# Kernel optimization log

Hardware: AMD Instinct MI355X
Metric: run time of the kernel (lower is better)

The kernel has to match this reference:

```python
import jax, jax.numpy as jnp
import numpy as np

B, S, D, H, L = 8, 1024, 768, 12, 8
DH = D // H
V, NCOND, DPA, NACT = 1024, 256, 64, 4
COND = DPA * NACT  # 256


def setup_inputs() -> dict:
    key = jax.random.key(0)
    ks = jax.random.split(key, 24)
    s = 0.02
    return {
        "tokens": jax.random.randint(ks[0], (B, S), 0, V),
        "actions": jax.random.randint(ks[1], (B, NACT), 0, NCOND),
        "emb": jax.random.normal(ks[2], (V, D)) * s,
        "act_emb": jax.random.normal(ks[3], (NCOND, DPA)) * s,
        "ln1_g": jax.random.normal(ks[4], (L, COND, D)) * s,
        "ln1_b": jax.random.normal(ks[5], (L, COND, D)) * s,
        "Wq": jax.random.normal(ks[6], (L, H, DH, DH)) * s,
        "Wk": jax.random.normal(ks[7], (L, H, DH, DH)) * s,
        "Wv": jax.random.normal(ks[8], (L, H, DH, DH)) * s,
        "Wo": jax.random.normal(ks[9], (L, D, D)) * s,
        "bo": jnp.zeros((L, D)),
        "ln2_g": jax.random.normal(ks[10], (L, COND, D)) * s,
        "ln2_b": jax.random.normal(ks[11], (L, COND, D)) * s,
        "W1": jax.random.normal(ks[12], (L, D, 4 * D)) * s,
        "b1": jnp.zeros((L, 4 * D)),
        "W2": jax.random.normal(ks[13], (L, 4 * D, D)) * s,
        "b2": jnp.zeros((L, D)),
        "lnf_g": jax.random.normal(ks[14], (COND, D)) * s,
        "lnf_b": jax.random.normal(ks[15], (COND, D)) * s,
        "Wout": jax.random.normal(ks[16], (D, V)) * s,
        "bout": jnp.zeros((V,)),
    }


def _sinusoidal_pe():
    pos = jnp.arange(S, dtype=jnp.float32)[:, None]
    div = jnp.exp(jnp.arange(0, D, 2, dtype=jnp.float32) * (-np.log(10000.0) / D))
    pe = jnp.zeros((S, D))
    pe = pe.at[:, 0::2].set(jnp.sin(pos * div))
    pe = pe.at[:, 1::2].set(jnp.cos(pos * div))
    return pe


def _cond_ln(x, a, gw, bw, eps=1e-5):
    # affine-free layernorm, conditional gain/shift from action vector (VideoGPT-style CondLayerNorm)
    mu = x.mean(-1, keepdims=True)
    var = ((x - mu) ** 2).mean(-1, keepdims=True)
    h = (x - mu) * jax.lax.rsqrt(var + eps)
    g = a @ gw  # [B, D]
    b = a @ bw
    return h * g[:, None, :] + b[:, None, :]


def _attn(h, wq, wk, wv, wo, bo_):
    xh = h.reshape(B, S, H, DH)
    q = jnp.einsum("bshd,hde->bshe", xh, wq)
    k = jnp.einsum("bshd,hde->bshe", xh, wk)
    v = jnp.einsum("bshd,hde->bshe", xh, wv)
    logits = jnp.einsum("bshe,bthe->bhst", q, k) / np.sqrt(DH)  # d_model per head = DH
    p = jax.nn.softmax(logits, axis=-1)
    o = jnp.einsum("bhst,bthd->bshd", p, v).reshape(B, S, D)
    return o @ wo + bo_


def reference(tokens, actions, emb, act_emb, ln1_g, ln1_b, Wq, Wk, Wv, Wo, bo,
              ln2_g, ln2_b, W1, b1, W2, b2, lnf_g, lnf_b, Wout, bout):
    x = emb[tokens] + _sinusoidal_pe()[None]  # [B, S, D]
    a = act_emb[actions].reshape(B, -1)  # first_action_only -> [B, COND]
    for l in range(L):
        h = _cond_ln(x, a, ln1_g[l], ln1_b[l])
        x = x + _attn(h, Wq[l], Wk[l], Wv[l], Wo[l], bo[l])
        h = _cond_ln(x, a, ln2_g[l], ln2_b[l])
        h = jax.nn.gelu(h @ W1[l] + b1[l]) @ W2[l] + b2[l]
        x = x + h
    x = _cond_ln(x, a, lnf_g, lnf_b)
    return x @ Wout + bout
```

## Files before the change

kernel.cpp:

```cpp
#include <hip/hip_runtime.h>
#include <hip/hip_bf16.h>

typedef unsigned short u16;
typedef __attribute__((ext_vector_type(8))) short bf16x8;
typedef __attribute__((ext_vector_type(4))) float f32x4;

#define NB 8
#define NS 1024
#define ND 768
#define NH 12
#define NL 8
#define NDH 64
#define NV 1024
#define NCONDV 256
#define NTOK (NB*NS)

union BF8 { bf16x8 v; u16 u[8]; };
union US4 { ushort4 v; u16 u[4]; };

__device__ __forceinline__ float b2f(u16 u){ return __uint_as_float(((unsigned)u) << 16); }
__device__ __forceinline__ u16 f2b(float f){
  unsigned u = __float_as_uint(f);
  return (u16)((u + 0x7fffu + ((u >> 16) & 1u)) >> 16);
}

__device__ __forceinline__ void glds16(const u16* g, u16* l) {
  __builtin_amdgcn_global_load_lds((const __attribute__((address_space(1))) void*)g,
                                   (__attribute__((address_space(3))) void*)l, 16, 0, 0);
}

#define MEMFENCE asm volatile("" ::: "memory")

__global__ __launch_bounds__(256) void k_embed(const int* __restrict__ tokens,
                                               const float* __restrict__ emb,
                                               float* __restrict__ x)
{
  const int t = blockIdx.x;
  const int s = t & (NS - 1);
  const int tok = tokens[t];
  const float c = (float)(-9.210340371976184 / 768.0);
  for (int d = threadIdx.x; d < ND; d += 256) {
    float div = expf((float)(d & ~1) * c);
    float ang = (float)s * div;
    float pe = (d & 1) ? cosf(ang) : sinf(ang);
    x[(size_t)t*ND + d] = emb[(size_t)tok*ND + d] + pe;
  }
}

__global__ __launch_bounds__(256) void k_actvec(const int* __restrict__ actions,
                                                const float* __restrict__ act_emb,
                                                float* __restrict__ a)
{
  const int b = blockIdx.x, j = threadIdx.x;
  const int i = j >> 6, kk = j & 63;
  const int act = actions[b*4 + i];
  a[b*NCONDV + j] = act_emb[(size_t)act*64 + kk];
}

__global__ __launch_bounds__(256) void k_gains(const float* __restrict__ a,
    const float* __restrict__ g1, const float* __restrict__ b1,
    const float* __restrict__ g2, const float* __restrict__ b2,
    const float* __restrict__ gf, const float* __restrict__ bfp,
    float* __restrict__ outp)
{
  __shared__ float sa[NB*NCONDV];
  const int m = blockIdx.x, dc = blockIdx.y;
  for (int i = threadIdx.x; i < NB*NCONDV; i += 256) sa[i] = a[i];
  __syncthreads();
  const float* W;
  if (m < 32) {
    int ll = m >> 2, w = m & 3;
    const float* base = (w==0) ? g1 : (w==1) ? b1 : (w==2) ? g2 : b2;
    W = base + (size_t)ll * NCONDV * ND;
  } else {
    W = (m == 32) ? gf : bfp;
  }
  const int d = dc*256 + threadIdx.x;
  float acc[NB] = {0,0,0,0,0,0,0,0};
  for (int j = 0; j < NCONDV; j++) {
    float w = W[(size_t)j*ND + d];
    #pragma unroll
    for (int bb = 0; bb < NB; bb++) acc[bb] += sa[bb*NCONDV + j] * w;
  }
  #pragma unroll
  for (int bb = 0; bb < NB; bb++) outp[((size_t)m*NB + bb)*ND + d] = acc[bb];
}

__global__ __launch_bounds__(256) void k_cln(const float* __restrict__ x,
                                             const float* __restrict__ g,
                                             const float* __restrict__ bb,
                                             u16* __restrict__ h)
{
  const int tid = threadIdx.x, w = tid >> 6, lane = tid & 63;
  const int t = blockIdx.x*4 + w;
  const int bi = t >> 10;
  const float* xr = x + (size_t)t*ND;
  f32x4 v0 = *(const f32x4*)(xr + lane*4);
  f32x4 v1 = *(const f32x4*)(xr + 256 + lane*4);
  f32x4 v2 = *(const f32x4*)(xr + 512 + lane*4);
  float s = (v0[0]+v0[1]+v0[2]+v0[3]) + (v1[0]+v1[1]+v1[2]+v1[3]) + (v2[0]+v2[1]+v2[2]+v2[3]);
  #pragma unroll
  for (int off = 1; off < 64; off <<= 1) s += __shfl_xor(s, off);
  float mu = s * (1.0f/768.0f);
  float s2 = 0.f;
  #pragma unroll
  for (int i = 0; i < 4; i++) { v0[i] -= mu; s2 += v0[i]*v0[i]; }
  #pragma unroll
  for (int i = 0; i < 4; i++) { v1[i] -= mu; s2 += v1[i]*v1[i]; }
  #pragma unroll
  for (int i = 0; i < 4; i++) { v2[i] -= mu; s2 += v2[i]*v2[i]; }
  #pragma unroll
  for (int off = 1; off < 64; off <<= 1) s2 += __shfl_xor(s2, off);
  float rs = rsqrtf(s2 * (1.0f/768.0f) + 1e-5f);
  const float* gr = g + (size_t)bi*ND;
  const float* br = bb + (size_t)bi*ND;
  u16* hr = h + (size_t)t*ND;
  #pragma unroll
  for (int j = 0; j < 3; j++) {
    f32x4 vv = (j==0) ? v0 : (j==1) ? v1 : v2;
    f32x4 gg = *(const f32x4*)(gr + j*256 + lane*4);
    f32x4 bv = *(const f32x4*)(br + j*256 + lane*4);
    US4 o;
    #pragma unroll
    for (int i = 0; i < 4; i++) o.u[i] = f2b(vv[i]*rs*gg[i] + bv[i]);
    *(ushort4*)(hr + j*256 + lane*4) = o.v;
  }
}

__global__ __launch_bounds__(256) void k_wprep(const float* __restrict__ src,
                                               u16* __restrict__ dst, int K, int N)
{
  __shared__ u16 t[64][65];
  const int k0 = blockIdx.x*64, n0 = blockIdx.y*64;
  const size_t mz = (size_t)blockIdx.z * K * N;
  src += mz; dst += mz;
  {
    int r = threadIdx.x >> 2, c0 = (threadIdx.x & 3) * 16;
    const float* s = src + (size_t)(k0 + r)*N + n0 + c0;
    f32x4 a = *(const f32x4*)s, b = *(const f32x4*)(s+4);
    f32x4 c = *(const f32x4*)(s+8), d = *(const f32x4*)(s+12);
    #pragma unroll
    for (int i = 0; i < 4; i++) {
      t[r][c0+i]    = f2b(a[i]);
      t[r][c0+4+i]  = f2b(b[i]);
      t[r][c0+8+i]  = f2b(c[i]);
      t[r][c0+12+i] = f2b(d[i]);
    }
  }
  __syncthreads();
  {
    int rn = threadIdx.x >> 2, kc = (threadIdx.x & 3)*16;
    u16* dp = dst + (size_t)(n0+rn)*K + k0 + kc;
    BF8 o0, o1;
    #pragma unroll
    for (int i = 0; i < 8; i++) { o0.u[i] = t[kc+i][rn]; o1.u[i] = t[kc+8+i][rn]; }
    *(bf16x8*)dp = o0.v; *(bf16x8*)(dp+8) = o1.v;
  }
}

__global__ __launch_bounds__(256) void k_qkv(const u16* __restrict__ h,
    const float* __restrict__ Wq, const float* __restrict__ Wk, const float* __restrict__ Wv,
    u16* __restrict__ qo, u16* __restrict__ ko, u16* __restrict__ vo)
{
  __shared__ alignas(16) u16 wlds[64][72];
  const int t0 = blockIdx.x * 64, head = blockIdx.y, which = blockIdx.z;
  const float* W = ((which==0) ? Wq : (which==1) ? Wk : Wv) + (size_t)head*NDH*NDH;
  {
    int d = threadIdx.x >> 2, e0 = (threadIdx.x & 3) * 16;
    const float* wr = W + (size_t)d*NDH + e0;
    f32x4 f0 = *(const f32x4*)wr;
    f32x4 f1 = *(const f32x4*)(wr + 4);
    f32x4 f2 = *(const f32x4*)(wr + 8);
    f32x4 f3 = *(const f32x4*)(wr + 12);
    #pragma unroll
    for (int i = 0; i < 4; i++) {
      wlds[e0+i][d]    = f2b(f0[i]);
      wlds[e0+4+i][d]  = f2b(f1[i]);
      wlds[e0+8+i][d]  = f2b(f2[i]);
      wlds[e0+12+i][d] = f2b(f3[i]);
    }
  }
  __syncthreads();
  const int wave = threadIdx.x >> 6, lane = threadIdx.x & 63;
  const int lo16 = lane & 15, quad = lane >> 4;
  const int arow = t0 + wave*16 + lo16;
  const u16* hr = h + (size_t)arow*ND + head*NDH + quad*8;
  bf16x8 a0 = *(const bf16x8*)hr;
  bf16x8 a1 = *(const bf16x8*)(hr + 32);
  f32x4 acc[4] = {{0,0,0,0},{0,0,0,0},{0,0,0,0},{0,0,0,0}};
  #pragma unroll
  for (int n = 0; n < 4; n++) {
    const u16* bp = &wlds[n*16 + lo16][quad*8];
    bf16x8 b0 = *(const bf16x8*)bp;
    bf16x8 b1 = *(const bf16x8*)(bp + 32);
    acc[n] = __builtin_amdgcn_mfma_f32_16x16x32_bf16(a0, b0, acc[n], 0, 0, 0);
    acc[n] = __builtin_amdgcn_mfma_f32_16x16x32_bf16(a1, b1, acc[n], 0, 0, 0);
  }
  #pragma unroll
  for (int n = 0; n < 4; n++) {
    #pragma unroll
    for (int r = 0; r < 4; r++) {
      int t = t0 + wave*16 + quad*4 + r;
      int bb = t >> 10, s = t & (NS-1);
      int e = n*16 + lo16;
      u16 val = f2b(acc[n][r]);
      if (which == 2) {
        int local = s & 127;
        int col = (s & ~127) | (((local & 15) << 3) | (local >> 4));
        vo[(((size_t)bb*NH + head)*NDH + e)*NS + col] = val;
      } else {
        u16* dst = (which == 0) ? qo : ko;
        dst[(((size_t)bb*NH + head)*NS + s)*NDH + e] = val;
      }
    }
  }
}

__global__ __launch_bounds__(256) void k_attn2(const u16* __restrict__ q,
                                               const u16* __restrict__ kk,
                                               const u16* __restrict__ vt,
                                               u16* __restrict__ o)
{
  __shared__ alignas(16) u16 klds[128][72];
  __shared__ alignas(16) u16 vlds[64][136];
  __shared__ alignas(16) u16 plds[4][16][136];
  const int tid = threadIdx.x, w = tid >> 6, lane = tid & 63;
  const int lo16 = lane & 15, quad = lane >> 4;
  const int bh = blockIdx.x;
  const int b = bh / NH, head = bh - b*NH;
  const int q0 = blockIdx.y*64 + w*16;
  const u16* qb = q  + (size_t)bh*NS*NDH;
  const u16* kb = kk + (size_t)bh*NS*NDH;
  const u16* vb = vt + (size_t)bh*NDH*NS;
  BF8 aq0, aq1;
  {
    const u16* qr = qb + (size_t)(q0 + lo16)*NDH + quad*8;
    BF8 r0, r1; r0.v = *(const bf16x8*)qr; r1.v = *(const bf16x8*)(qr + 32);
    const float qs = 0.125f * 1.44269504088896f;
    #pragma unroll
    for (int j = 0; j < 8; j++) {
      aq0.u[j] = f2b(b2f(r0.u[j]) * qs);
      aq1.u[j] = f2b(b2f(r1.u[j]) * qs);
    }
  }
  float lsum[4] = {0,0,0,0};
  f32x4 oacc[4] = {{0,0,0,0},{0,0,0,0},{0,0,0,0},{0,0,0,0}};

  bf16x8 kreg[4], vreg[4];
  #pragma unroll
  for (int i = 0; i < 4; i++) {
    int c = tid + 256*i;
    kreg[i] = *(const bf16x8*)(kb + (size_t)(c>>3)*NDH + (c&7)*8);
    vreg[i] = *(const bf16x8*)(vb + (size_t)(c>>4)*NS + (c&15)*8);
  }

  for (int kt = 0; kt < NS; kt += 128) {
    __syncthreads();
    #pragma unroll
    for (int i = 0; i < 4; i++) {
      int c = tid + 256*i;
      *(bf16x8*)&klds[c>>3][(c&7)*8] = kreg[i];
      *(bf16x8*)&vlds[c>>4][(c&15)*8] = vreg[i];
    }
    __syncthreads();
    if (kt + 128 < NS) {
      #pragma unroll
      for (int i = 0; i < 4; i++) {
        int c = tid + 256*i;
        kreg[i] = *(const bf16x8*)(kb + (size_t)(kt + 128 + (c>>3))*NDH + (c&7)*8);
        vreg[i] = *(const bf16x8*)(vb + (size_t)(c>>4)*NS + (kt + 128) + (c&15)*8);
      }
    }
    f32x4 s[8];
    #pragma unroll
    for (int j = 0; j < 8; j++) {
      const u16* kr = &klds[j*16 + lo16][quad*8];
      bf16x8 b0 = *(const bf16x8*)kr;
      bf16x8 b1 = *(const bf16x8*)(kr + 32);
      f32x4 z = {0,0,0,0};
      z = __builtin_amdgcn_mfma_f32_16x16x32_bf16(aq0.v, b0, z, 0, 0, 0);
      s[j] = __builtin_amdgcn_mfma_f32_16x16x32_bf16(aq1.v, b1, z, 0, 0, 0);
    }
    #pragma unroll
    for (int r = 0; r < 4; r++) {
      float p[8];
      #pragma unroll
      for (int j = 0; j < 8; j++) p[j] = exp2f(s[j][r]);
      unsigned pk32[4];
      #pragma unroll
      for (int j = 0; j < 4; j++)
        asm("v_cvt_pk_bf16_f32 %0, %1, %2" : "=v"(pk32[j]) : "v"(p[2*j]), "v"(p[2*j+1]));
      float ps = 0.f;
      #pragma unroll
      for (int j = 0; j < 4; j++) {
        ps += __uint_as_float(pk32[j] << 16);
        ps += __uint_as_float(pk32[j] & 0xffff0000u);
      }
      lsum[r] += ps;
      union { unsigned u[4]; bf16x8 v; } pkv;
      #pragma unroll
      for (int j = 0; j < 4; j++) pkv.u[j] = pk32[j];
      *(bf16x8*)&plds[w][quad*4 + r][lo16*8] = pkv.v;
    }
    #pragma unroll
    for (int kc = 0; kc < 4; kc++) {
      bf16x8 pa = *(const bf16x8*)&plds[w][lo16][kc*32 + quad*8];
      #pragma unroll
      for (int n = 0; n < 4; n++) {
        bf16x8 vf = *(const bf16x8*)&vlds[n*16 + lo16][kc*32 + quad*8];
        oacc[n] = __builtin_amdgcn_mfma_f32_16x16x32_bf16(pa, vf, oacc[n], 0, 0, 0);
      }
    }
  }
  #pragma unroll
  for (int r = 0; r < 4; r++) {
    #pragma unroll
    for (int off = 1; off < 16; off <<= 1) lsum[r] += __shfl_xor(lsum[r], off);
  }
  #pragma unroll
  for (int n = 0; n < 4; n++) {
    #pragma unroll
    for (int r = 0; r < 4; r++) {
      int s_ = q0 + quad*4 + r;
      int d = head*NDH + n*16 + lo16;
      o[((size_t)b*NS + s_)*ND + d] = f2b(oacc[n][r] / lsum[r]);
    }
  }
}

template<int EPI>
__global__ __launch_bounds__(512) void k_gemm3(
    const u16* __restrict__ A, const u16* __restrict__ Bt,
    const float* __restrict__ bias, const float* __restrict__ resid,
    void* __restrict__ out, int M, int N, int K)
{
  extern __shared__ u16 lds[];
  const int tid = threadIdx.x;
  const int lane = tid & 63, lo16 = lane & 15, quad = lane >> 4;
  const int w = tid >> 6;
  const int wm = (w & 3) << 6;
  const int wn = (w >> 2) << 6;

  const int nwg = (int)gridDim.x, flat = (int)blockIdx.x;
  const int swzid = (flat & 7) * (nwg >> 3) + (flat >> 3);
  const int nbn = N >> 7;
  const int mb = swzid / nbn, nb = swzid - mb*nbn;
  const int m0 = mb << 8, n0 = nb << 7;
  const int NT = K >> 6;

  const int sr = tid >> 3, ss = tid & 7;
  const int sg = ((ss ^ (sr & 7)) << 3);
  const u16* Asrc = A + (size_t)(m0 + sr) * K + sg;
  const u16* Bsrc = Bt + (size_t)(n0 + sr) * K + sg;
  const size_t K64 = (size_t)K << 6;
  u16* const sd = lds + tid * 8;

  const int sw0 = ((quad ^ (lo16 & 7)) << 3);
  const int sw1 = (((4 + quad) ^ (lo16 & 7)) << 3);
  const int arow = (wm + lo16) << 6;
  const int brow = (wn + lo16) << 6;

  f32x4 acc[4][4];
  #pragma unroll
  for (int i = 0; i < 4; i++)
    #pragma unroll
    for (int j = 0; j < 4; j++) acc[i][j] = (f32x4){0,0,0,0};

  auto STAGE = [&](int t, int bi) {
    u16* dst = sd + bi * 24576;
    const size_t ko = (size_t)t << 6;
    #pragma unroll
    for (int c = 0; c < 4; c++) glds16(Asrc + ko + (size_t)c*K64, dst + c*4096);
    #pragma unroll
    for (int c = 0; c < 2; c++) glds16(Bsrc + ko + (size_t)c*K64, dst + 16384 + c*4096);
  };

  STAGE(0, 0);
  if (NT > 1) STAGE(1, 1);

  int cu = 0;
  for (int t = 0; t < NT; t++) {
    const int st = (cu == 0) ? 2 : cu - 1;
    MEMFENCE; __builtin_amdgcn_s_barrier(); MEMFENCE;
    if (t + 2 < NT) {
      STAGE(t + 2, st);
      asm volatile("s_waitcnt vmcnt(12)" ::: "memory");
    } else if (t + 1 < NT) {
      asm volatile("s_waitcnt vmcnt(6)" ::: "memory");
    } else {
      asm volatile("s_waitcnt vmcnt(0)" ::: "memory");
    }
    MEMFENCE; __builtin_amdgcn_s_barrier(); MEMFENCE;
    const u16* cb = lds + cu * 24576;
    bf16x8 af[4][2], bf[4][2];
    #pragma unroll
    for (int mf = 0; mf < 4; mf++) {
      af[mf][0] = *(const bf16x8*)(cb + arow + mf*1024 + sw0);
      af[mf][1] = *(const bf16x8*)(cb + arow + mf*1024 + sw1);
    }
    #pragma unroll
    for (int nf = 0; nf < 4; nf++) {
      bf[nf][0] = *(const bf16x8*)(cb + 16384 + brow + nf*1024 + sw0);
      bf[nf][1] = *(const bf16x8*)(cb + 16384 + brow + nf*1024 + sw1);
    }
    __builtin_amdgcn_s_setprio(1);
    #pragma unroll
    for (int kk = 0; kk < 2; kk++)
      #pragma unroll
      for (int mf = 0; mf < 4; mf++)
        #pragma unroll
        for (int nf = 0; nf < 4; nf++)
          acc[mf][nf] = __builtin_amdgcn_mfma_f32_16x16x32_bf16(af[mf][kk], bf[nf][kk], acc[mf][nf], 0, 0, 0);
    __builtin_amdgcn_s_setprio(0);
    cu = (cu == 2) ? 0 : cu + 1;
  }

  #pragma unroll
  for (int mf = 0; mf < 4; mf++) {
    #pragma unroll
    for (int nf = 0; nf < 4; nf++) {
      const int col = n0 + wn + nf*16 + lo16;
      const float bv = bias[col];
      #pragma unroll
      for (int r = 0; r < 4; r++) {
        const int row = m0 + wm + mf*16 + quad*4 + r;
        const size_t idx = (size_t)row * N + col;
        float v = acc[mf][nf][r] + bv;
        if (EPI == 1) {
          float u = 0.7978845608028654f*(v + 0.044715f*v*v*v);
          float e = __expf(2.0f*u);
          float th = (e - 1.0f) / (e + 1.0f);
          ((u16*)out)[idx] = f2b(0.5f*v*(1.0f + th));
        } else if (EPI == 2) {
          ((float*)out)[idx] = v + resid[idx];
        } else {
          ((float*)out)[idx] = v;
        }
      }
    }
  }
}

template<int EPI, int MT>
__global__ __launch_bounds__(256) void k_gemm_t(
    const u16* __restrict__ A, const u16* __restrict__ Bt,
    const float* __restrict__ bias, const float* resid,
    void* out, int M, int N, int K)
{
  constexpr int MI = MT/32;
  __shared__ alignas(16) u16 alds[2*MT*32];
  __shared__ alignas(16) u16 blds[2*128*32];
  const int m0 = blockIdx.x*MT, n0 = blockIdx.y*128;
  const int tid = threadIdx.x;
  const int w = tid >> 6, lane = tid & 63, lo16 = lane & 15, quad = lane >> 4;
  const int wm = (w & 1)*(MT/2), wn = (w >> 1)*64;
  f32x4 acc[MI][4];
  #pragma unroll
  for (int i = 0; i < MI; i++)
    #pragma unroll
    for (int j = 0; j < 4; j++) acc[i][j] = (f32x4){0,0,0,0};
  const int r0 = tid >> 2, c0 = (tid & 3)*8;
  const u16* Ap = A  + (size_t)(m0 + r0)*K + c0;
  const u16* Bp = Bt + (size_t)(n0 + r0)*K + c0;
  for (int k0 = 0; k0 < K; k0 += 64) {
    __syncthreads();
    #pragma unroll
    for (int h = 0; h < 2; h++) {
      const int ho = h*32;
      glds16(Ap + k0 + ho, alds + h*(MT*32) + tid*8);
      if (MT == 128) glds16(Ap + (size_t)64*K + k0 + ho, alds + h*(MT*32) + 2048 + tid*8);
      glds16(Bp + k0 + ho, blds + h*4096 + tid*8);
      glds16(Bp + (size_t)64*K + k0 + ho, blds + h*4096 + 2048 + tid*8);
    }
    __syncthreads();
    #pragma unroll
    for (int h = 0; h < 2; h++) {
      const u16* ah = alds + h*(MT*32);
      const u16* bh = blds + h*4096;
      bf16x8 af[MI], bf[4];
      #pragma unroll
      for (int i = 0; i < MI; i++) af[i] = *(const bf16x8*)&ah[(wm + i*16 + lo16)*32 + quad*8];
      #pragma unroll
      for (int j = 0; j < 4; j++) bf[j] = *(const bf16x8*)&bh[(wn + j*16 + lo16)*32 + quad*8];
      #pragma unroll
      for (int i = 0; i < MI; i++)
        #pragma unroll
        for (int j = 0; j < 4; j++)
          acc[i][j] = __builtin_amdgcn_mfma_f32_16x16x32_bf16(af[i], bf[j], acc[i][j], 0, 0, 0);
    }
  }
  #pragma unroll
  for (int j = 0; j < 4; j++) {
    int col = n0 + wn + j*16 + lo16;
    float bv = bias[col];
    #pragma unroll
    for (int i = 0; i < MI; i++) {
      #pragma unroll
      for (int r = 0; r < 4; r++) {
        int row = m0 + wm + i*16 + quad*4 + r;
        float v = acc[i][j][r] + bv;
        if (EPI == 1) {
          float u = 0.7978845608028654f*(v + 0.044715f*v*v*v);
          float e = __expf(2.0f*u);
          float th = (e - 1.0f) / (e + 1.0f);
          ((u16*)out)[(size_t)row*N + col] = f2b(0.5f*v*(1.0f + th));
        } else if (EPI == 2) {
          ((float*)out)[(size_t)row*N + col] = v + resid[(size_t)row*N + col];
        } else {
          ((float*)out)[(size_t)row*N + col] = v;
        }
      }
    }
  }
}

template<int EPI>
__global__ __launch_bounds__(256) void k_gemm(
    const u16* __restrict__ A, const float* __restrict__ Bw,
    const float* __restrict__ bias, const float* resid,
    void* out, int M, int N, int K)
{
  __shared__ alignas(16) u16 alds[64][40];
  __shared__ alignas(16) u16 blds[64][40];
  const int m0 = blockIdx.x * 64, n0b = blockIdx.y * 64;
  const int tid = threadIdx.x;
  const int wave = tid >> 6, lane = tid & 63, lo16 = lane & 15, quad = lane >> 4;
  f32x4 acc[4] = {{0,0,0,0},{0,0,0,0},{0,0,0,0},{0,0,0,0}};
  const int ar = tid >> 2, ac = (tid & 3) * 8;
  const int bk = tid >> 3, bn = (tid & 7) * 8;
  for (int k0 = 0; k0 < K; k0 += 32) {
    __syncthreads();
    *(bf16x8*)&alds[ar][ac] = *(const bf16x8*)(A + (size_t)(m0+ar)*K + k0 + ac);
    {
      const float* brow = Bw + (size_t)(k0+bk)*N + n0b + bn;
      f32x4 f0 = *(const f32x4*)brow;
      f32x4 f1 = *(const f32x4*)(brow + 4);
      #pragma unroll
      for (int i = 0; i < 4; i++) {
        blds[bn+i][bk]   = f2b(f0[i]);
        blds[bn+4+i][bk] = f2b(f1[i]);
      }
    }
    __syncthreads();
    bf16x8 af = *(const bf16x8*)&alds[wave*16 + lo16][quad*8];
    #pragma unroll
    for (int n = 0; n < 4; n++) {
      bf16x8 bf = *(const bf16x8*)&blds[n*16 + lo16][quad*8];
      acc[n] = __builtin_amdgcn_mfma_f32_16x16x32_bf16(af, bf, acc[n], 0, 0, 0);
    }
  }
  const int rbase = m0 + wave*16 + quad*4;
  #pragma unroll
  for (int n = 0; n < 4; n++) {
    int col = n0b + n*16 + lo16;
    float bv = bias[col];
    #pragma unroll
    for (int r = 0; r < 4; r++) {
      int row = rbase + r;
      float v = acc[n][r] + bv;
      if (EPI == 1) {
        float x3 = v*v*v;
        v = 0.5f*v*(1.0f + tanhf(0.7978845608028654f*(v + 0.044715f*x3)));
        ((u16*)out)[(size_t)row*N + col] = f2b(v);
      } else if (EPI == 2) {
        ((float*)out)[(size_t)row*N + col] = v + resid[(size_t)row*N + col];
      } else {
        ((float*)out)[(size_t)row*N + col] = v;
      }
    }
  }
}

extern "C" void kernel_launch(void* const* d_in, const int* in_sizes, int n_in,
                              void* d_out, int out_size, void* d_ws, size_t ws_size,
                              hipStream_t stream)
{
  (void)in_sizes; (void)n_in; (void)out_size;
  const int*   tokens  = (const int*)d_in[0];
  const int*   actions = (const int*)d_in[1];
  const float* emb     = (const float*)d_in[2];
  const float* act_emb = (const float*)d_in[3];
  const float* ln1_g   = (const float*)d_in[4];
  const float* ln1_b   = (const float*)d_in[5];
  const float* Wq      = (const float*)d_in[6];
  const float* Wk      = (const float*)d_in[7];
  const float* Wv      = (const float*)d_in[8];
  const float* Wo      = (const float*)d_in[9];
  const float* bo      = (const float*)d_in[10];
  const float* ln2_g   = (const float*)d_in[11];
  const float* ln2_b   = (const float*)d_in[12];
  const float* W1      = (const float*)d_in[13];
  const float* b1      = (const float*)d_in[14];
  const float* W2      = (const float*)d_in[15];
  const float* b2      = (const float*)d_in[16];
  const float* lnf_g   = (const float*)d_in[17];
  const float* lnf_b   = (const float*)d_in[18];
  const float* Wout    = (const float*)d_in[19];
  const float* bout    = (const float*)d_in[20];

  char* p = (char*)d_ws;
  float* abuf = (float*)p;  p += (size_t)NB*NCONDV*4;
  float* gbuf = (float*)p;  p += (size_t)34*NB*ND*4;
  float* xbuf = (float*)p;  p += (size_t)NTOK*ND*4;
  u16*   hbuf = (u16*)p;    p += (size_t)NTOK*ND*2;
  u16*   region = (u16*)p;
  u16* qbuf = region;
  u16* kbuf = region + (size_t)NTOK*ND;
  u16* vbuf = region + (size_t)2*NTOK*ND;
  u16* obuf = (u16*)d_out;

  size_t base = (size_t)(p - (char*)d_ws) + (size_t)3*NTOK*ND*2;
  size_t hid_sz = (size_t)NTOK*3072*2;
  size_t woT_sz = (size_t)NL*ND*ND*2;
  size_t w1T_sz = (size_t)NL*ND*3072*2;
  size_t w2T_sz = (size_t)NL*3072*ND*2;
  size_t woutT_sz = (size_t)ND*NV*2;
  size_t req_fast = base + hid_sz + woT_sz + w1T_sz + w2T_sz + woutT_sz;
  const bool fast = (ws_size >= req_fast);

  static int g8 = -1;
  if (g8 < 0) {
    bool ok = true;
    ok = ok && (hipFuncSetAttribute(reinterpret_cast<const void*>(k_gemm3<0>),
                hipFuncAttributeMaxDynamicSharedMemorySize, 147456) == hipSuccess);
    ok = ok && (hipFuncSetAttribute(reinterpret_cast<const void*>(k_gemm3<1>),
                hipFuncAttributeMaxDynamicSharedMemorySize, 147456) == hipSuccess);
    ok = ok && (hipFuncSetAttribute(reinterpret_cast<const void*>(k_gemm3<2>),
                hipFuncAttributeMaxDynamicSharedMemorySize, 147456) == hipSuccess);
    g8 = ok ? 1 : 0;
  }

  k_embed <<<NTOK, 256, 0, stream>>>(tokens, emb, xbuf);
  k_actvec<<<NB, 256, 0, stream>>>(actions, act_emb, abuf);
  k_gains <<<dim3(34,3), 256, 0, stream>>>(abuf, ln1_g, ln1_b, ln2_g, ln2_b, lnf_g, lnf_b, gbuf);

  if (fast) {
    char* q2 = (char*)d_ws + base;
    u16* hidbuf = (u16*)q2;  q2 += hid_sz;
    u16* WoT   = (u16*)q2;   q2 += woT_sz;
    u16* W1T   = (u16*)q2;   q2 += w1T_sz;
    u16* W2T   = (u16*)q2;   q2 += w2T_sz;
    u16* WoutT = (u16*)q2;

    k_wprep<<<dim3(ND/64, ND/64, NL), 256, 0, stream>>>(Wo, WoT, ND, ND);
    k_wprep<<<dim3(ND/64, 3072/64, NL), 256, 0, stream>>>(W1, W1T, ND, 3072);
    k_wprep<<<dim3(3072/64, ND/64, NL), 256, 0, stream>>>(W2, W2T, 3072, ND);
    k_wprep<<<dim3(ND/64, NV/64, 1), 256, 0, stream>>>(Wout, WoutT, ND, NV);

    for (int l = 0; l < NL; l++) {
      k_cln<<<NTOK/4, 256, 0, stream>>>(xbuf, gbuf + (size_t)(l*4+0)*NB*ND, gbuf + (size_t)(l*4+1)*NB*ND, hbuf);
      k_qkv<<<dim3(NTOK/64, NH, 3), 256, 0, stream>>>(hbuf,
          Wq + (size_t)l*NH*NDH*NDH, Wk + (size_t)l*NH*NDH*NDH, Wv + (size_t)l*NH*NDH*NDH,
          qbuf, kbuf, vbuf);
      k_attn2<<<dim3(NB*NH, NS/64), 256, 0, stream>>>(qbuf, kbuf, vbuf, obuf);
      if (g8) {
        k_gemm3<2><<<dim3((NTOK/256)*(ND/128)), 512, 147456, stream>>>(
            obuf, WoT + (size_t)l*ND*ND, bo + (size_t)l*ND, xbuf, xbuf, NTOK, ND, ND);
      } else {
        k_gemm_t<2,64><<<dim3(NTOK/64, ND/128), 256, 0, stream>>>(obuf, WoT + (size_t)l*ND*ND,
            bo + (size_t)l*ND, xbuf, xbuf, NTOK, ND, ND);
      }
      k_cln<<<NTOK/4, 256, 0, stream>>>(xbuf, gbuf + (size_t)(l*4+2)*NB*ND, gbuf + (size_t)(l*4+3)*NB*ND, hbuf);
      if (g8) {
        k_gemm3<1><<<dim3((NTOK/256)*(3072/128)), 512, 147456, stream>>>(
            hbuf, W1T + (size_t)l*ND*3072, b1 + (size_t)l*3072, nullptr, hidbuf, NTOK, 3072, ND);
        k_gemm3<2><<<dim3((NTOK/256)*(ND/128)), 512, 147456, stream>>>(
            hidbuf, W2T + (size_t)l*3072*ND, b2 + (size_t)l*ND, xbuf, xbuf, NTOK, ND, 3072);
      } else {
        k_gemm_t<1,128><<<dim3(NTOK/128, 3072/128), 256, 0, stream>>>(hbuf, W1T + (size_t)l*ND*3072,
            b1 + (size_t)l*3072, nullptr, hidbuf, NTOK, 3072, ND);
        k_gemm_t<2,64><<<dim3(NTOK/64, ND/128), 256, 0, stream>>>(hidbuf, W2T + (size_t)l*3072*ND,
            b2 + (size_t)l*ND, xbuf, xbuf, NTOK, ND, 3072);
      }
    }
    k_cln<<<NTOK/4, 256, 0, stream>>>(xbuf, gbuf + (size_t)32*NB*ND, gbuf + (size_t)33*NB*ND, hbuf);
    if (g8) {
      k_gemm3<0><<<dim3((NTOK/256)*(NV/128)), 512, 147456, stream>>>(
          hbuf, WoutT, bout, nullptr, (float*)d_out, NTOK, NV, ND);
    } else {
      k_gemm_t<0,64><<<dim3(NTOK/64, NV/128), 256, 0, stream>>>(hbuf, WoutT, bout, nullptr, (float*)d_out, NTOK, NV, ND);
    }
  } else {
    u16* hidbuf = region;
    for (int l = 0; l < NL; l++) {
      k_cln<<<NTOK/4, 256, 0, stream>>>(xbuf, gbuf + (size_t)(l*4+0)*NB*ND, gbuf + (size_t)(l*4+1)*NB*ND, hbuf);
      k_qkv<<<dim3(NTOK/64, NH, 3), 256, 0, stream>>>(hbuf,
          Wq + (size_t)l*NH*NDH*NDH, Wk + (size_t)l*NH*NDH*NDH, Wv + (size_t)l*NH*NDH*NDH,
          qbuf, kbuf, vbuf);
      k_attn2<<<dim3(NB*NH, NS/64), 256, 0, stream>>>(qbuf, kbuf, vbuf, obuf);
      k_gemm<2><<<dim3(NTOK/64, ND/64), 256, 0, stream>>>(obuf, Wo + (size_t)l*ND*ND,
          bo + (size_t)l*ND, xbuf, xbuf, NTOK, ND, ND);
      k_cln<<<NTOK/4, 256, 0, stream>>>(xbuf, gbuf + (size_t)(l*4+2)*NB*ND, gbuf + (size_t)(l*4+3)*NB*ND, hbuf);
      for (int c = 0; c < 2; c++) {
        const size_t mo = (size_t)c * 4096;
        k_gemm<1><<<dim3(4096/64, 3072/64), 256, 0, stream>>>(hbuf + mo*ND, W1 + (size_t)l*ND*3072,
            b1 + (size_t)l*3072, nullptr, hidbuf, 4096, 3072, ND);
        k_gemm<2><<<dim3(4096/64, ND/64), 256, 0, stream>>>(hidbuf, W2 + (size_t)l*3072*ND,
            b2 + (size_t)l*ND, xbuf + mo*ND, xbuf + mo*ND, 4096, ND, 3072);
      }
    }
    k_cln<<<NTOK/4, 256, 0, stream>>>(xbuf, gbuf + (size_t)32*NB*ND, gbuf + (size_t)33*NB*ND, hbuf);
    k_gemm<0><<<dim3(NTOK/64, NV/64), 256, 0, stream>>>(hbuf, Wout, bout, nullptr, (float*)d_out, NTOK, NV, ND);
  }
}
```

Measured before the change: 2.386 ms.

## Add 256x256-tile double-buffered GEMM kernel for the W1 GELU projection

Adds a new GEMM kernel with 256x256 output tiles and 8 waves, each computing a 128x64 sub-tile, with a K-step of 64 and two LDS buffers. It is used only for the FFN up-projection with the GELU epilogue. Each output tile now gets more arithmetic per byte loaded, which cuts global and LDS traffic per MFMA. The cost is a large accumulator (128 floats per lane), which risks register pressure and lower occupancy. The grid also shrinks to 384 workgroups on 256 CUs, so the last wave of workgroups is unbalanced.

```diff
diff --git a/kernel.cpp b/kernel.cpp
--- a/kernel.cpp
+++ b/kernel.cpp
@@ -324,6 +324,122 @@
       int s_ = q0 + quad*4 + r;
       int d = head*NDH + n*16 + lo16;
       o[((size_t)b*NS + s_)*ND + d] = f2b(oacc[n][r] / lsum[r]);
+    }
+  }
+}
+
+template<int EPI>
+__global__ __launch_bounds__(512) void k_gemm4(
+    const u16* __restrict__ A, const u16* __restrict__ Bt,
+    const float* __restrict__ bias, const float* __restrict__ resid,
+    void* __restrict__ out, int M, int N, int K)
+{
+  extern __shared__ u16 lds[];
+  const int tid = threadIdx.x;
+  const int lane = tid & 63, lo16 = lane & 15, quad = lane >> 4;
+  const int w = tid >> 6;
+  const int wm = (w >> 2) << 7;
+  const int wn = (w & 3) << 6;
+
+  const int nwg = (int)gridDim.x, flat = (int)blockIdx.x;
+  const int swzid = ((nwg & 7) == 0) ? ((flat & 7) * (nwg >> 3) + (flat >> 3)) : flat;
+  const int nbn = N >> 8;
+  const int mb = swzid / nbn, nb = swzid - mb*nbn;
+  const int m0 = mb << 8, n0 = nb << 8;
+  const int NT = K >> 6;
+
+  const int sr = tid >> 3, ss = tid & 7;
+  const int sg = ((ss ^ (sr & 7)) << 3);
+  const u16* Asrc = A + (size_t)(m0 + sr) * K + sg;
+  const u16* Bsrc = Bt + (size_t)(n0 + sr) * K + sg;
+  const size_t K64 = (size_t)K << 6;
+  u16* const sd = lds + tid * 8;
+
+  const int sw0 = ((quad ^ (lo16 & 7)) << 3);
+  const int sw1 = (((4 + quad) ^ (lo16 & 7)) << 3);
+  const int arow = (wm + lo16) << 6;
+  const int brow = (wn + lo16) << 6;
+
+  float bv[4];
+  #pragma unroll
+  for (int nf = 0; nf < 4; nf++) {
+    bv[nf] = bias[n0 + wn + nf*16 + lo16];
+    asm volatile("" :: "v"(bv[nf]));
+  }
+
+  f32x4 acc[8][4];
+  #pragma unroll
+  for (int i = 0; i < 8; i++)
+    #pragma unroll
+    for (int j = 0; j < 4; j++) acc[i][j] = (f32x4){0,0,0,0};
+
+  auto STAGE = [&](int t, int bi) {
+    u16* dst = sd + bi * 32768;
+    const size_t ko = (size_t)t << 6;
+    #pragma unroll
+    for (int c = 0; c < 4; c++) glds16(Asrc + ko + (size_t)c*K64, dst + c*4096);
+    #pragma unroll
+    for (int c = 0; c < 4; c++) glds16(Bsrc + ko + (size_t)c*K64, dst + 16384 + c*4096);
+  };
+
+  STAGE(0, 0);
+  for (int t = 0; t < NT; t++) {
+    MEMFENCE; __builtin_amdgcn_s_barrier(); MEMFENCE;
+    if (t + 1 < NT) {
+      STAGE(t + 1, (t + 1) & 1);
+      asm volatile("s_waitcnt vmcnt(8)" ::: "memory");
+    } else {
+      asm volatile("s_waitcnt vmcnt(0)" ::: "memory");
+    }
+    MEMFENCE; __builtin_amdgcn_s_barrier(); MEMFENCE;
+    const u16* cb = lds + (t & 1) * 32768;
+    bf16x8 bfr[4][2];
+    #pragma unroll
+    for (int nf = 0; nf < 4; nf++) {
+      bfr[nf][0] = *(const bf16x8*)(cb + 16384 + brow + nf*1024 + sw0);
+      bfr[nf][1] = *(const bf16x8*)(cb + 16384 + brow + nf*1024 + sw1);
+    }
+    #pragma unroll
+    for (int mh = 0; mh < 2; mh++) {
+      bf16x8 af[4][2];
+      #pragma unroll
+      for (int mf = 0; mf < 4; mf++) {
+        af[mf][0] = *(const bf16x8*)(cb + arow + (mh*4+mf)*1024 + sw0);
+        af[mf][1] = *(const bf16x8*)(cb + arow + (mh*4+mf)*1024 + sw1);
+      }
+      __builtin_amdgcn_s_setprio(1);
+      #pragma unroll
+      for (int kk = 0; kk < 2; kk++)
+        #pragma unroll
+        for (int mf = 0; mf < 4; mf++)
+          #pragma unroll
+          for (int nf = 0; nf < 4; nf++)
+            acc[mh*4+mf][nf] = __builtin_amdgcn_mfma_f32_16x16x32_bf16(af[mf][kk], bfr[nf][kk], acc[mh*4+mf][nf], 0, 0, 0);
+      __builtin_amdgcn_s_setprio(0);
+    }
+  }
+
+  #pragma unroll
+  for (int fi = 0; fi < 8; fi++) {
+    #pragma unroll
+    for (int nf = 0; nf < 4; nf++) {
+      const int col = n0 + wn + nf*16 + lo16;
+      #pragma unroll
+      for (int r = 0; r < 4; r++) {
+        const int row = m0 + wm + fi*16 + quad*4 + r;
+        const size_t idx = (size_t)row * N + col;
+        float v = acc[fi][nf][r] + bv[nf];
+        if (EPI == 1) {
+          float u = 0.7978845608028654f*(v + 0.044715f*v*v*v);
+          float e = __expf(2.0f*u);
+          float th = (e - 1.0f) / (e + 1.0f);
+          ((u16*)out)[idx] = f2b(0.5f*v*(1.0f + th));
+        } else if (EPI == 2) {
+          ((float*)out)[idx] = v + resid[idx];
+        } else {
+          ((float*)out)[idx] = v;
+        }
+      }
     }
   }
 }
@@ -627,6 +743,8 @@
                 hipFuncAttributeMaxDynamicSharedMemorySize, 147456) == hipSuccess);
     ok = ok && (hipFuncSetAttribute(reinterpret_cast<const void*>(k_gemm3<2>),
                 hipFuncAttributeMaxDynamicSharedMemorySize, 147456) == hipSuccess);
+    ok = ok && (hipFuncSetAttribute(reinterpret_cast<const void*>(k_gemm4<1>),
+                hipFuncAttributeMaxDynamicSharedMemorySize, 131072) == hipSuccess);
     g8 = ok ? 1 : 0;
   }
 
@@ -662,7 +780,7 @@
       }
       k_cln<<<NTOK/4, 256, 0, stream>>>(xbuf, gbuf + (size_t)(l*4+2)*NB*ND, gbuf + (size_t)(l*4+3)*NB*ND, hbuf);
       if (g8) {
-        k_gemm3<1><<<dim3((NTOK/256)*(3072/128)), 512, 147456, stream>>>(
+        k_gemm4<1><<<dim3((NTOK/256)*(3072/256)), 512, 131072, stream>>>(
             hbuf, W1T + (size_t)l*ND*3072, b1 + (size_t)l*3072, nullptr, hidbuf, NTOK, 3072, ND);
         k_gemm3<2><<<dim3((NTOK/256)*(ND/128)), 512, 147456, stream>>>(
             hidbuf, W2T + (size_t)l*3072*ND, b2 + (size_t)l*ND, xbuf, xbuf, NTOK, ND, 3072);
```

Result: slower. 2.445 ms (+2.5%).

## Replace 256x128 triple-buffered GEMM with 128x128 double-buffered kernel and fuse QKV

Applied to the files above, without the earlier changes.

The dense GEMMs move from a 512-thread, 256x128-tile, three-stage pipeline using 144KB of dynamic LDS to a 256-thread, 128x128-tile, two-stage pipeline with 64KB of static LDS. Bias is loaded into registers before the main loop, and the hipFuncSetAttribute path and fallback kernel are removed. The QKV kernel now computes all three projections in one block, so the activation tile is loaded once instead of three times. The GEMM change gives more blocks and possibly higher occupancy but a shallower prefetch and less reuse per tile.

```diff
diff --git a/kernel.cpp b/kernel.cpp
--- a/kernel.cpp
+++ b/kernel.cpp
@@ -162,22 +162,25 @@
     const float* __restrict__ Wq, const float* __restrict__ Wk, const float* __restrict__ Wv,
     u16* __restrict__ qo, u16* __restrict__ ko, u16* __restrict__ vo)
 {
-  __shared__ alignas(16) u16 wlds[64][72];
-  const int t0 = blockIdx.x * 64, head = blockIdx.y, which = blockIdx.z;
-  const float* W = ((which==0) ? Wq : (which==1) ? Wk : Wv) + (size_t)head*NDH*NDH;
+  __shared__ alignas(16) u16 wlds[3][64][72];
+  const int t0 = blockIdx.x * 64, head = blockIdx.y;
   {
     int d = threadIdx.x >> 2, e0 = (threadIdx.x & 3) * 16;
-    const float* wr = W + (size_t)d*NDH + e0;
-    f32x4 f0 = *(const f32x4*)wr;
-    f32x4 f1 = *(const f32x4*)(wr + 4);
-    f32x4 f2 = *(const f32x4*)(wr + 8);
-    f32x4 f3 = *(const f32x4*)(wr + 12);
-    #pragma unroll
-    for (int i = 0; i < 4; i++) {
-      wlds[e0+i][d]    = f2b(f0[i]);
-      wlds[e0+4+i][d]  = f2b(f1[i]);
-      wlds[e0+8+i][d]  = f2b(f2[i]);
-      wlds[e0+12+i][d] = f2b(f3[i]);
+    #pragma unroll
+    for (int which = 0; which < 3; which++) {
+      const float* W = ((which==0) ? Wq : (which==1) ? Wk : Wv) + (size_t)head*NDH*NDH;
+      const float* wr = W + (size_t)d*NDH + e0;
+      f32x4 f0 = *(const f32x4*)wr;
+      f32x4 f1 = *(const f32x4*)(wr + 4);
+      f32x4 f2 = *(const f32x4*)(wr + 8);
+      f32x4 f3 = *(const f32x4*)(wr + 12);
+      #pragma unroll
+      for (int i = 0; i < 4; i++) {
+        wlds[which][e0+i][d]    = f2b(f0[i]);
+        wlds[which][e0+4+i][d]  = f2b(f1[i]);
+        wlds[which][e0+8+i][d]  = f2b(f2[i]);
+        wlds[which][e0+12+i][d] = f2b(f3[i]);
+      }
     }
   }
   __syncthreads();
@@ -187,30 +190,33 @@
   const u16* hr = h + (size_t)arow*ND + head*NDH + quad*8;
   bf16x8 a0 = *(const bf16x8*)hr;
   bf16x8 a1 = *(const bf16x8*)(hr + 32);
-  f32x4 acc[4] = {{0,0,0,0},{0,0,0,0},{0,0,0,0},{0,0,0,0}};
-  #pragma unroll
-  for (int n = 0; n < 4; n++) {
-    const u16* bp = &wlds[n*16 + lo16][quad*8];
-    bf16x8 b0 = *(const bf16x8*)bp;
-    bf16x8 b1 = *(const bf16x8*)(bp + 32);
-    acc[n] = __builtin_amdgcn_mfma_f32_16x16x32_bf16(a0, b0, acc[n], 0, 0, 0);
-    acc[n] = __builtin_amdgcn_mfma_f32_16x16x32_bf16(a1, b1, acc[n], 0, 0, 0);
-  }
-  #pragma unroll
-  for (int n = 0; n < 4; n++) {
-    #pragma unroll
-    for (int r = 0; r < 4; r++) {
-      int t = t0 + wave*16 + quad*4 + r;
-      int bb = t >> 10, s = t & (NS-1);
-      int e = n*16 + lo16;
-      u16 val = f2b(acc[n][r]);
-      if (which == 2) {
-        int local = s & 127;
-        int col = (s & ~127) | (((local & 15) << 3) | (local >> 4));
-        vo[(((size_t)bb*NH + head)*NDH + e)*NS + col] = val;
-      } else {
-        u16* dst = (which == 0) ? qo : ko;
-        dst[(((size_t)bb*NH + head)*NS + s)*NDH + e] = val;
+  #pragma unroll
+  for (int which = 0; which < 3; which++) {
+    f32x4 acc[4] = {{0,0,0,0},{0,0,0,0},{0,0,0,0},{0,0,0,0}};
+    #pragma unroll
+    for (int n = 0; n < 4; n++) {
+      const u16* bp = &wlds[which][n*16 + lo16][quad*8];
+      bf16x8 b0 = *(const bf16x8*)bp;
+      bf16x8 b1 = *(const bf16x8*)(bp + 32);
+      acc[n] = __builtin_amdgcn_mfma_f32_16x16x32_bf16(a0, b0, acc[n], 0, 0, 0);
+      acc[n] = __builtin_amdgcn_mfma_f32_16x16x32_bf16(a1, b1, acc[n], 0, 0, 0);
+    }
+    #pragma unroll
+    for (int n = 0; n < 4; n++) {
+      #pragma unroll
+      for (int r = 0; r < 4; r++) {
+        int t = t0 + wave*16 + quad*4 + r;
+        int bb = t >> 10, s = t & (NS-1);
+        int e = n*16 + lo16;
+        u16 val = f2b(acc[n][r]);
+        if (which == 2) {
+          int local = s & 127;
+          int col = (s & ~127) | (((local & 15) << 3) | (local >> 4));
+          vo[(((size_t)bb*NH + head)*NDH + e)*NS + col] = val;
+        } else {
+          u16* dst = (which == 0) ? qo : ko;
+          dst[(((size_t)bb*NH + head)*NS + s)*NDH + e] = val;
+        }
       }
     }
   }
@@ -329,30 +335,30 @@
 }
 
 template<int EPI>
-__global__ __launch_bounds__(512) void k_gemm3(
+__global__ __launch_bounds__(256) void k_gemm6(
     const u16* __restrict__ A, const u16* __restrict__ Bt,
     const float* __restrict__ bias, const float* __restrict__ resid,
     void* __restrict__ out, int M, int N, int K)
 {
-  extern __shared__ u16 lds[];
+  __shared__ alignas(16) u16 lds[2*16384];
   const int tid = threadIdx.x;
   const int lane = tid & 63, lo16 = lane & 15, quad = lane >> 4;
   const int w = tid >> 6;
-  const int wm = (w & 3) << 6;
-  const int wn = (w >> 2) << 6;
+  const int wm = (w & 1) << 6;
+  const int wn = (w >> 1) << 6;
 
   const int nwg = (int)gridDim.x, flat = (int)blockIdx.x;
-  const int swzid = (flat & 7) * (nwg >> 3) + (flat >> 3);
+  const int swzid = ((nwg & 7) == 0) ? ((flat & 7) * (nwg >> 3) + (flat >> 3)) : flat;
   const int nbn = N >> 7;
   const int mb = swzid / nbn, nb = swzid - mb*nbn;
-  const int m0 = mb << 8, n0 = nb << 7;
+  const int m0 = mb << 7, n0 = nb << 7;
   const int NT = K >> 6;
 
   const int sr = tid >> 3, ss = tid & 7;
   const int sg = ((ss ^ (sr & 7)) << 3);
   const u16* Asrc = A + (size_t)(m0 + sr) * K + sg;
   const u16* Bsrc = Bt + (size_t)(n0 + sr) * K + sg;
-  const size_t K64 = (size_t)K << 6;
+  const size_t K32 = (size_t)K << 5;
   u16* const sd = lds + tid * 8;
 
   const int sw0 = ((quad ^ (lo16 & 7)) << 3);
@@ -360,6 +366,13 @@
   const int arow = (wm + lo16) << 6;
   const int brow = (wn + lo16) << 6;
 
+  float bv[4];
+  #pragma unroll
+  for (int nf = 0; nf < 4; nf++) {
+    bv[nf] = bias[n0 + wn + nf*16 + lo16];
+    asm volatile("" :: "v"(bv[nf]));
+  }
+
   f32x4 acc[4][4];
   #pragma unroll
   for (int i = 0; i < 4; i++)
@@ -367,31 +380,25 @@
     for (int j = 0; j < 4; j++) acc[i][j] = (f32x4){0,0,0,0};
 
   auto STAGE = [&](int t, int bi) {
-    u16* dst = sd + bi * 24576;
+    u16* dst = sd + bi * 16384;
     const size_t ko = (size_t)t << 6;
     #pragma unroll
-    for (int c = 0; c < 4; c++) glds16(Asrc + ko + (size_t)c*K64, dst + c*4096);
-    #pragma unroll
-    for (int c = 0; c < 2; c++) glds16(Bsrc + ko + (size_t)c*K64, dst + 16384 + c*4096);
+    for (int c = 0; c < 4; c++) glds16(Asrc + ko + (size_t)c*K32, dst + c*2048);
+    #pragma unroll
+    for (int c = 0; c < 4; c++) glds16(Bsrc + ko + (size_t)c*K32, dst + 8192 + c*2048);
   };
 
   STAGE(0, 0);
-  if (NT > 1) STAGE(1, 1);
-
-  int cu = 0;
   for (int t = 0; t < NT; t++) {
-    const int st = (cu == 0) ? 2 : cu - 1;
     MEMFENCE; __builtin_amdgcn_s_barrier(); MEMFENCE;
-    if (t + 2 < NT) {
-      STAGE(t + 2, st);
-      asm volatile("s_waitcnt vmcnt(12)" ::: "memory");
-    } else if (t + 1 < NT) {
-      asm volatile("s_waitcnt vmcnt(6)" ::: "memory");
+    if (t + 1 < NT) {
+      STAGE(t + 1, (t + 1) & 1);
+      asm volatile("s_waitcnt vmcnt(8)" ::: "memory");
     } else {
       asm volatile("s_waitcnt vmcnt(0)" ::: "memory");
     }
     MEMFENCE; __builtin_amdgcn_s_barrier(); MEMFENCE;
-    const u16* cb = lds + cu * 24576;
+    const u16* cb = lds + (t & 1) * 16384;
     bf16x8 af[4][2], bf[4][2];
     #pragma unroll
     for (int mf = 0; mf < 4; mf++) {
@@ -400,8 +407,8 @@
     }
     #pragma unroll
     for (int nf = 0; nf < 4; nf++) {
-      bf[nf][0] = *(const bf16x8*)(cb + 16384 + brow + nf*1024 + sw0);
-      bf[nf][1] = *(const bf16x8*)(cb + 16384 + brow + nf*1024 + sw1);
+      bf[nf][0] = *(const bf16x8*)(cb + 8192 + brow + nf*1024 + sw0);
+      bf[nf][1] = *(const bf16x8*)(cb + 8192 + brow + nf*1024 + sw1);
     }
     __builtin_amdgcn_s_setprio(1);
     #pragma unroll
@@ -412,7 +419,6 @@
         for (int nf = 0; nf < 4; nf++)
           acc[mf][nf] = __builtin_amdgcn_mfma_f32_16x16x32_bf16(af[mf][kk], bf[nf][kk], acc[mf][nf], 0, 0, 0);
     __builtin_amdgcn_s_setprio(0);
-    cu = (cu == 2) ? 0 : cu + 1;
   }
 
   #pragma unroll
@@ -420,12 +426,11 @@
     #pragma unroll
     for (int nf = 0; nf < 4; nf++) {
       const int col = n0 + wn + nf*16 + lo16;
-      const float bv = bias[col];
       #pragma unroll
       for (int r = 0; r < 4; r++) {
         const int row = m0 + wm + mf*16 + quad*4 + r;
         const size_t idx = (size_t)row * N + col;
-        float v = acc[mf][nf][r] + bv;
+        float v = acc[mf][nf][r] + bv[nf];
         if (EPI == 1) {
           float u = 0.7978845608028654f*(v + 0.044715f*v*v*v);
           float e = __expf(2.0f*u);
@@ -435,79 +440,6 @@
           ((float*)out)[idx] = v + resid[idx];
         } else {
           ((float*)out)[idx] = v;
-        }
-      }
-    }
-  }
-}
-
-template<int EPI, int MT>
-__global__ __launch_bounds__(256) void k_gemm_t(
-    const u16* __restrict__ A, const u16* __restrict__ Bt,
-    const float* __restrict__ bias, const float* resid,
-    void* out, int M, int N, int K)
-{
-  constexpr int MI = MT/32;
-  __shared__ alignas(16) u16 alds[2*MT*32];
-  __shared__ alignas(16) u16 blds[2*128*32];
-  const int m0 = blockIdx.x*MT, n0 = blockIdx.y*128;
-  const int tid = threadIdx.x;
-  const int w = tid >> 6, lane = tid & 63, lo16 = lane & 15, quad = lane >> 4;
-  const int wm = (w & 1)*(MT/2), wn = (w >> 1)*64;
-  f32x4 acc[MI][4];
-  #pragma unroll
-  for (int i = 0; i < MI; i++)
-    #pragma unroll
-    for (int j = 0; j < 4; j++) acc[i][j] = (f32x4){0,0,0,0};
-  const int r0 = tid >> 2, c0 = (tid & 3)*8;
-  const u16* Ap = A  + (size_t)(m0 + r0)*K + c0;
-  const u16* Bp = Bt + (size_t)(n0 + r0)*K + c0;
-  for (int k0 = 0; k0 < K; k0 += 64) {
-    __syncthreads();
-    #pragma unroll
-    for (int h = 0; h < 2; h++) {
-      const int ho = h*32;
-      glds16(Ap + k0 + ho, alds + h*(MT*32) + tid*8);
-      if (MT == 128) glds16(Ap + (size_t)64*K + k0 + ho, alds + h*(MT*32) + 2048 + tid*8);
-      glds16(Bp + k0 + ho, blds + h*4096 + tid*8);
-      glds16(Bp + (size_t)64*K + k0 + ho, blds + h*4096 + 2048 + tid*8);
-    }
-    __syncthreads();
-    #pragma unroll
-    for (int h = 0; h < 2; h++) {
-      const u16* ah = alds + h*(MT*32);
-      const u16* bh = blds + h*4096;
-      bf16x8 af[MI], bf[4];
-      #pragma unroll
-      for (int i = 0; i < MI; i++) af[i] = *(const bf16x8*)&ah[(wm + i*16 + lo16)*32 + quad*8];
-      #pragma unroll
-      for (int j = 0; j < 4; j++) bf[j] = *(const bf16x8*)&bh[(wn + j*16 + lo16)*32 + quad*8];
-      #pragma unroll
-      for (int i = 0; i < MI; i++)
-        #pragma unroll
-        for (int j = 0; j < 4; j++)
-          acc[i][j] = __builtin_amdgcn_mfma_f32_16x16x32_bf16(af[i], bf[j], acc[i][j], 0, 0, 0);
-    }
-  }
-  #pragma unroll
-  for (int j = 0; j < 4; j++) {
-    int col = n0 + wn + j*16 + lo16;
-    float bv = bias[col];
-    #pragma unroll
-    for (int i = 0; i < MI; i++) {
-      #pragma unroll
-      for (int r = 0; r < 4; r++) {
-        int row = m0 + wm + i*16 + quad*4 + r;
-        float v = acc[i][j][r] + bv;
-        if (EPI == 1) {
-          float u = 0.7978845608028654f*(v + 0.044715f*v*v*v);
-          float e = __expf(2.0f*u);
-          float th = (e - 1.0f) / (e + 1.0f);
-          ((u16*)out)[(size_t)row*N + col] = f2b(0.5f*v*(1.0f + th));
-        } else if (EPI == 2) {
-          ((float*)out)[(size_t)row*N + col] = v + resid[(size_t)row*N + col];
-        } else {
-          ((float*)out)[(size_t)row*N + col] = v;
         }
       }
     }
@@ -618,18 +550,6 @@
   size_t req_fast = base + hid_sz + woT_sz + w1T_sz + w2T_sz + woutT_sz;
   const bool fast = (ws_size >= req_fast);
 
-  static int g8 = -1;
-  if (g8 < 0) {
-    bool ok = true;
-    ok = ok && (hipFuncSetAttribute(reinterpret_cast<const void*>(k_gemm3<0>),
-                hipFuncAttributeMaxDynamicSharedMemorySize, 147456) == hipSuccess);
-    ok = ok && (hipFuncSetAttribute(reinterpret_cast<const void*>(k_gemm3<1>),
-                hipFuncAttributeMaxDynamicSharedMemorySize, 147456) == hipSuccess);
-    ok = ok && (hipFuncSetAttribute(reinterpret_cast<const void*>(k_gemm3<2>),
-                hipFuncAttributeMaxDynamicSharedMemorySize, 147456) == hipSuccess);
-    g8 = ok ? 1 : 0;
-  }
-
   k_embed <<<NTOK, 256, 0, stream>>>(tokens, emb, xbuf);
   k_actvec<<<NB, 256, 0, stream>>>(actions, act_emb, abuf);
   k_gains <<<dim3(34,3), 256, 0, stream>>>(abuf, ln1_g, ln1_b, ln2_g, ln2_b, lnf_g, lnf_b, gbuf);
@@ -649,42 +569,26 @@
 
     for (int l = 0; l < NL; l++) {
       k_cln<<<NTOK/4, 256, 0, stream>>>(xbuf, gbuf + (size_t)(l*4+0)*NB*ND, gbuf + (size_t)(l*4+1)*NB*ND, hbuf);
-      k_qkv<<<dim3(NTOK/64, NH, 3), 256, 0, stream>>>(hbuf,
+      k_qkv<<<dim3(NTOK/64, NH), 256, 0, stream>>>(hbuf,
           Wq + (size_t)l*NH*NDH*NDH, Wk + (size_t)l*NH*NDH*NDH, Wv + (size_t)l*NH*NDH*NDH,
           qbuf, kbuf, vbuf);
       k_attn2<<<dim3(NB*NH, NS/64), 256, 0, stream>>>(qbuf, kbuf, vbuf, obuf);
-      if (g8) {
-        k_gemm3<2><<<dim3((NTOK/256)*(ND/128)), 512, 147456, stream>>>(
-            obuf, WoT + (size_t)l*ND*ND, bo + (size_t)l*ND, xbuf, xbuf, NTOK, ND, ND);
-      } else {
-        k_gemm_t<2,64><<<dim3(NTOK/64, ND/128), 256, 0, stream>>>(obuf, WoT + (size_t)l*ND*ND,
-            bo + (size_t)l*ND, xbuf, xbuf, NTOK, ND, ND);
-      }
+      k_gemm6<2><<<dim3((NTOK/128)*(ND/128)), 256, 0, stream>>>(
+          obuf, WoT + (size_t)l*ND*ND, bo + (size_t)l*ND, xbuf, xbuf, NTOK, ND, ND);
       k_cln<<<NTOK/4, 256, 0, stream>>>(xbuf, gbuf + (size_t)(l*4+2)*NB*ND, gbuf + (size_t)(l*4+3)*NB*ND, hbuf);
-      if (g8) {
-        k_gemm3<1><<<dim3((NTOK/256)*(3072/128)), 512, 147456, stream>>>(
-            hbuf, W1T + (size_t)l*ND*3072, b1 + (size_t)l*3072, nullptr, hidbuf, NTOK, 3072, ND);
-        k_gemm3<2><<<dim3((NTOK/256)*(ND/128)), 512, 147456, stream>>>(
-            hidbuf, W2T + (size_t)l*3072*ND, b2 + (size_t)l*ND, xbuf, xbuf, NTOK, ND, 3072);
-      } else {
-        k_gemm_t<1,128><<<dim3(NTOK/128, 3072/128), 256, 0, stream>>>(hbuf, W1T + (size_t)l*ND*3072,
-            b1 + (size_t)l*3072, nullptr, hidbuf, NTOK, 3072, ND);
-        k_gemm_t<2,64><<<dim3(NTOK/64, ND/128), 256, 0, stream>>>(hidbuf, W2T + (size_t)l*3072*ND,
-            b2 + (size_t)l*ND, xbuf, xbuf, NTOK, ND, 3072);
-      }
+      k_gemm6<1><<<dim3((NTOK/128)*(3072/128)), 256, 0, stream>>>(
+          hbuf, W1T + (size_t)l*ND*3072, b1 + (size_t)l*3072, nullptr, hidbuf, NTOK, 3072, ND);
+      k_gemm6<2><<<dim3((NTOK/128)*(ND/128)), 256, 0, stream>>>(
+          hidbuf, W2T + (size_t)l*3072*ND, b2 + (size_t)l*ND, xbuf, xbuf, NTOK, ND, 3072);
     }
     k_cln<<<NTOK/4, 256, 0, stream>>>(xbuf, gbuf + (size_t)32*NB*ND, gbuf + (size_t)33*NB*ND, hbuf);
-    if (g8) {
-      k_gemm3<0><<<dim3((NTOK/256)*(NV/128)), 512, 147456, stream>>>(
-          hbuf, WoutT, bout, nullptr, (float*)d_out, NTOK, NV, ND);
-    } else {
-      k_gemm_t<0,64><<<dim3(NTOK/64, NV/128), 256, 0, stream>>>(hbuf, WoutT, bout, nullptr, (float*)d_out, NTOK, NV, ND);
-    }
+    k_gemm6<0><<<dim3((NTOK/128)*(NV/128)), 256, 0, stream>>>(
+        hbuf, WoutT, bout, nullptr, (float*)d_out, NTOK, NV, ND);
   } else {
     u16* hidbuf = region;
     for (int l = 0; l < NL; l++) {
       k_cln<<<NTOK/4, 256, 0, stream>>>(xbuf, gbuf + (size_t)(l*4+0)*NB*ND, gbuf + (size_t)(l*4+1)*NB*ND, hbuf);
-      k_qkv<<<dim3(NTOK/64, NH, 3), 256, 0, stream>>>(hbuf,
+      k_qkv<<<dim3(NTOK/64, NH), 256, 0, stream>>>(hbuf,
           Wq + (size_t)l*NH*NDH*NDH, Wk + (size_t)l*NH*NDH*NDH, Wv + (size_t)l*NH*NDH*NDH,
           qbuf, kbuf, vbuf);
       k_attn2<<<dim3(NB*NH, NS/64), 256, 0, stream>>>(qbuf, kbuf, vbuf, obuf);
```

Result: faster. 2.155 ms (-9.7%).
